# Kernel tuning notes

Hardware: AMD Instinct MI355X
Metric: run time of the kernel (lower is better)

The kernel has to match this reference:

```python
import jax, jax.numpy as jnp
import numpy as np

N, M_CHE, M_VDW, B = 20000, 20, 20, 200
H, E, NODE_IN, NCONV = 128, 20, 13, 3
CHE_CUTOFF, VDW_CUTOFF = 8.0, 12.0


def setup_inputs() -> dict:
    key = jax.random.key(0)
    ks = jax.random.split(key, 16)
    s = 0.05
    inp = {}
    inp['atoms_embed'] = jax.random.normal(ks[0], (N, NODE_IN), jnp.float32)
    inp['che_nbrs_fea'] = jax.random.uniform(ks[1], (N, M_CHE), jnp.float32, 0.5, CHE_CUTOFF * 1.1)
    inp['vdw_nbrs_fea'] = jax.random.uniform(ks[2], (N, M_VDW), jnp.float32, 0.5, VDW_CUTOFF * 1.1)
    inp['che_nbrs_idx'] = jax.random.randint(ks[3], (N, M_CHE), 0, N)
    inp['vdw_nbrs_idx'] = jax.random.randint(ks[4], (N, M_VDW), 0, N)
    inp['num_atoms'] = jnp.full((B,), N // B, dtype=jnp.int32)  # 200 crystals x 100 atoms
    inp['emb_W'] = jax.random.normal(ks[5], (NODE_IN, H), jnp.float32) * s
    inp['emb_b'] = jnp.zeros((H,), jnp.float32)
    inp['che_filter_W'] = jax.random.normal(ks[6], (NCONV, E, H), jnp.float32) * s
    inp['che_filter_b'] = jnp.zeros((NCONV, H), jnp.float32)
    inp['che_fc_W'] = jax.random.normal(ks[7], (NCONV, 3 * H, 2 * H), jnp.float32) * s
    inp['che_fc_b'] = jnp.zeros((NCONV, 2 * H), jnp.float32)
    inp['vdw_filter_W'] = jax.random.normal(ks[8], (NCONV, E, H), jnp.float32) * s
    inp['vdw_filter_b'] = jnp.zeros((NCONV, H), jnp.float32)
    inp['vdw_fc_W'] = jax.random.normal(ks[9], (NCONV, 3 * H, 2 * H), jnp.float32) * s
    inp['vdw_fc_b'] = jnp.zeros((NCONV, 2 * H), jnp.float32)
    inp['fc1_W'] = jax.random.normal(ks[10], (H, H), jnp.float32) * s
    inp['fc1_b'] = jnp.zeros((H,), jnp.float32)
    inp['out_W'] = jax.random.normal(ks[11], (H, 1), jnp.float32) * s
    inp['out_b'] = jnp.zeros((1,), jnp.float32)
    return inp


def _rbf(d, cutoff):
    # sinc-like radial basis with cosine envelope; zero beyond cutoff
    k = jnp.arange(1, E + 1, dtype=d.dtype)  # [E]
    de = d[..., None]  # [N, M, 1]
    r = jnp.where(de < cutoff, jnp.sin(de * k * (jnp.pi / cutoff)) / de, jnp.zeros((), d.dtype))
    env = 0.5 * (jnp.cos(jnp.pi * d / cutoff) + 1.0)
    return r * env[..., None]  # [N, M, E]


def _conv_half(nodes, rbf_e, idx, fW, fb, gW, gb):
    n, m = idx.shape
    edges = rbf_e @ fW + fb  # [N, M, H]
    self_fea = jnp.broadcast_to(nodes[:, None, :], (n, m, nodes.shape[1]))
    total = jnp.concatenate([self_fea, edges, nodes[idx]], axis=2)  # [N, M, 3H]
    gated = total @ gW + gb  # [N, M, 2H]
    filt, core = jnp.split(gated, 2, axis=2)
    return jnp.sum(jax.nn.sigmoid(filt) * jax.nn.softplus(core), axis=1)  # [N, H]


def reference(atoms_embed, che_nbrs_fea, che_nbrs_idx, vdw_nbrs_fea, vdw_nbrs_idx,
              num_atoms, emb_W, emb_b, che_filter_W, che_filter_b, che_fc_W, che_fc_b,
              vdw_filter_W, vdw_filter_b, vdw_fc_W, vdw_fc_b, fc1_W, fc1_b, out_W, out_b):
    nodes = atoms_embed @ emb_W + emb_b  # [N, H]
    che_rbf = _rbf(che_nbrs_fea, CHE_CUTOFF)
    vdw_rbf = _rbf(vdw_nbrs_fea, VDW_CUTOFF)
    for i in range(NCONV):
        che = _conv_half(nodes, che_rbf, che_nbrs_idx, che_filter_W[i], che_filter_b[i], che_fc_W[i], che_fc_b[i])
        vdw = _conv_half(nodes, vdw_rbf, vdw_nbrs_idx, vdw_filter_W[i], vdw_filter_b[i], vdw_fc_W[i], vdw_fc_b[i])
        nodes = jax.nn.softplus(nodes + che + vdw)
    # per-crystal mean pooling from contiguous atom ranges given by num_atoms
    ends = jnp.cumsum(num_atoms)
    seg = jnp.searchsorted(ends, jnp.arange(nodes.shape[0]), side='right')
    sums = jax.ops.segment_sum(nodes, seg, num_segments=B)
    crys = sums / num_atoms[:, None].astype(nodes.dtype)  # [B, H]
    crys = jax.nn.softplus(jax.nn.softplus(crys) @ fc1_W + fc1_b)
    predict = (crys @ out_W + out_b)[:, 0]  # [B]
    return predict
```

## Files before the change

kernel.cpp:

```cpp
#include <hip/hip_runtime.h>
#include <hip/hip_bf16.h>
#include <math.h>

#define NN 20000
#define MM 20
#define EE 20
#define HH 128
#define BB 200
#define NCONV 3
#define CHE_CUT 8.0f
#define VDW_CUT 12.0f
#define PI_F 3.14159265358979323846f
#define LOG2E_F 1.44269504088896340736f
#define LN2_F 0.69314718055994530942f

typedef __fp16 half2_t __attribute__((ext_vector_type(2)));
typedef __fp16 half4_t __attribute__((ext_vector_type(4)));
typedef _Float16 f16x8 __attribute__((ext_vector_type(8)));
typedef float f32x4 __attribute__((ext_vector_type(4)));

__device__ __forceinline__ float exp2_(float x) {
#if __has_builtin(__builtin_amdgcn_exp2f)
    return __builtin_amdgcn_exp2f(x);
#else
    return exp2f(x);
#endif
}
__device__ __forceinline__ float log2_(float x) {
#if __has_builtin(__builtin_amdgcn_logf)
    return __builtin_amdgcn_logf(x);
#else
    return log2f(x);
#endif
}
__device__ __forceinline__ float rcp_(float x) {
#if __has_builtin(__builtin_amdgcn_rcpf)
    return __builtin_amdgcn_rcpf(x);
#else
    return 1.f / x;
#endif
}
__device__ __forceinline__ float med3_(float a, float b, float c) {
#if __has_builtin(__builtin_amdgcn_fmed3f)
    return __builtin_amdgcn_fmed3f(a, b, c);
#else
    return fminf(a, fmaxf(b, c));
#endif
}
__device__ __forceinline__ float sp_(float x) {
    return (x > 15.f) ? x : LN2_F * log2_(1.f + exp2_(x * LOG2E_F));
}
__device__ __forceinline__ float fdot2_(half2_t a, half2_t b, float c) {
#if __has_builtin(__builtin_amdgcn_fdot2)
    return __builtin_amdgcn_fdot2(a, b, c, false);
#else
    return (float)a.x * (float)b.x + (float)a.y * (float)b.y + c;
#endif
}

__global__ void prep_bias(const float* __restrict__ cfb, const float* __restrict__ cgW,
                          const float* __restrict__ cgb,
                          const float* __restrict__ vfb, const float* __restrict__ vgW,
                          const float* __restrict__ vgb, float* __restrict__ bc) {
    int half = blockIdx.y;
    int l = blockIdx.z;
    int j = threadIdx.x;
    const float* fb = half ? vfb : cfb;
    const float* gW = half ? vgW : cgW;
    const float* gb = half ? vgb : cgb;
    const float* gWe = gW + ((size_t)l * 384 + 128) * 256;
    const float* brow = fb + (size_t)l * HH;
    float acc = gb[(size_t)l * 256 + j];
    for (int k = 0; k < HH; ++k) acc = fmaf(brow[k], gWe[k * 256 + j], acc);
    bc[((size_t)l * 2 + half) * 256 + j] = acc * LOG2E_F;
}

__global__ void prep_bwc(const float* __restrict__ cfW, const float* __restrict__ cgW,
                         const float* __restrict__ vfW, const float* __restrict__ vgW,
                         _Float16* __restrict__ bwc) {
    int nt = blockIdx.x;
    int half = blockIdx.y;
    int l = blockIdx.z;
    int tid = threadIdx.x;
    int k = tid >> 4, nc = tid & 15;
    int t = (nt & 7) * 16 + nc;
    int gcol = (nt >> 3) * 128 + t;
    const float* fW = half ? vfW : cfW;
    const float* gW = half ? vgW : cgW;
    const float* gWe = gW + ((size_t)l * 384 + 128) * 256;
    float val = 0.f;
    if (k < EE) {
        const float* frow = fW + ((size_t)l * EE + k) * HH;
        for (int kk = 0; kk < HH; ++kk) val = fmaf(frow[kk], gWe[kk * 256 + gcol], val);
        val *= LOG2E_F;
    }
    bwc[(((size_t)(l * 2 + half) * 16 + nt) * 64 + (k >> 3) * 16 + nc) * 8 + (k & 7)] = (_Float16)val;
}

__global__ void prep_bpk(const float* __restrict__ cgW, const float* __restrict__ vgW,
                         _Float16* __restrict__ bpk) {
    int i = blockIdx.x * 256 + threadIdx.x;
    if (i >= NCONV * 128 * 1024) return;
    int l = i >> 17;
    int rem = i & 131071;
    int k = rem >> 10;
    int c = rem & 1023;
    int half = (c >> 8) & 1;
    const float* src = half ? vgW : cgW;
    int grow = l * 384 + ((c < 512) ? k : 256 + k);
    float val = src[(size_t)grow * 256 + (c & 255)] * LOG2E_F;
    int nt = c >> 4, nc = c & 15;
    int s = k >> 5, kq = (k >> 3) & 3, j = k & 7;
    bpk[(size_t)l * 131072 + (((size_t)nt * 4 + s) * 64 + kq * 16 + nc) * 8 + j] = (_Float16)val;
}

__global__ void embed_kernel(const float* __restrict__ atoms, const float* __restrict__ W,
                             const float* __restrict__ bias, float* __restrict__ nodes,
                             _Float16* __restrict__ nodes_h) {
    int n = blockIdx.x, t = threadIdx.x;
    const float* arow = atoms + (size_t)n * 13;
    float acc = bias[t];
    #pragma unroll
    for (int k = 0; k < 13; ++k) acc = fmaf(arow[k], W[k * HH + t], acc);
    nodes[(size_t)n * HH + t] = acc;
    nodes_h[(size_t)n * HH + t] = (_Float16)acc;
}

__global__ void rbf_kernel(const float* __restrict__ che_fea, const float* __restrict__ vdw_fea,
                           _Float16* __restrict__ rfrag) {
    int i = blockIdx.x * blockDim.x + threadIdx.x;
    if (i >= 2 * NN * MM) return;
    bool isv = i >= NN * MM;
    int rem = isv ? i - NN * MM : i;
    int n = rem / MM, m = rem % MM;
    float d = isv ? vdw_fea[rem] : che_fea[rem];
    float cutoff = isv ? VDW_CUT : CHE_CUT;
    float x = d * (PI_F / cutoff);
    float s1 = sinf(x), c1 = cosf(x);
    float env = 0.5f * (c1 + 1.f);
    float scale = (d < cutoff) ? (env / d) : 0.f;
    float out[EE];
    float skm1 = 0.f, sk = s1;
    #pragma unroll
    for (int e = 0; e < EE; ++e) {
        out[e] = sk * scale;
        float nx = 2.f * c1 * sk - skm1;
        skm1 = sk; sk = nx;
    }
    _Float16* rf = rfrag + (size_t)(isv ? NN + n : n) * 640;
    f16x8 v0, v1, v2, v3;
    #pragma unroll
    for (int j = 0; j < 8; ++j) {
        v0[j] = (_Float16)out[j];
        v1[j] = (_Float16)out[8 + j];
        v2[j] = (j < 4) ? (_Float16)out[16 + j] : (_Float16)0.f;
        v3[j] = (_Float16)0.f;
    }
    if (m < 16) {
        _Float16* base = rf + m * 8;
        *(f16x8*)(base) = v0;
        *(f16x8*)(base + 128) = v1;
        *(f16x8*)(base + 256) = v2;
        *(f16x8*)(base + 384) = v3;
    } else {
        _Float16* base = rf + 512 + (m - 16) * 8;
        *(f16x8*)(base) = v0;
        *(f16x8*)(base + 32) = v1;
        *(f16x8*)(base + 64) = v2;
        *(f16x8*)(base + 96) = v3;
    }
}

__global__ __launch_bounds__(256)
void gemm_mfma(const _Float16* __restrict__ Ah, const _Float16* __restrict__ Bpk,
               half2_t* __restrict__ Spk, half2_t* __restrict__ Ypk) {
    int lane = threadIdx.x & 63;
    int wv = threadIdx.x >> 6;
    int m0 = blockIdx.x * 32;
    int la = lane & 15;
    int quad = lane >> 4;
    int k0 = quad * 8;

    f16x8 af0[4], af1[4];
    {
        const _Float16* arow = Ah + (size_t)(m0 + la) * 128 + k0;
        #pragma unroll
        for (int s = 0; s < 4; ++s) {
            af0[s] = *(const f16x8*)(arow + s * 32);
            af1[s] = *(const f16x8*)(arow + 2048 + s * 32);
        }
    }

    const f16x8* bp = (const f16x8*)Bpk;
    int ntf0 = wv * 16;
    half2_t* dst = (wv & 2) ? Ypk : Spk;
    int wbase = (wv & 1) * 128 + la;

    f16x8 fb[4], cb[4], nfb[4], ncb[4];
    #pragma unroll
    for (int s = 0; s < 4; ++s) {
        fb[s] = bp[((size_t)ntf0 * 4 + s) * 64 + lane];
        cb[s] = bp[((size_t)(ntf0 + 8) * 4 + s) * 64 + lane];
    }
    for (int p = 0; p < 8; ++p) {
        if (p < 7) {
            #pragma unroll
            for (int s = 0; s < 4; ++s) {
                nfb[s] = bp[((size_t)(ntf0 + p + 1) * 4 + s) * 64 + lane];
                ncb[s] = bp[((size_t)(ntf0 + 9 + p) * 4 + s) * 64 + lane];
            }
        }
        f32x4 a0f = {0.f, 0.f, 0.f, 0.f};
        f32x4 a0c = {0.f, 0.f, 0.f, 0.f};
        f32x4 a1f = {0.f, 0.f, 0.f, 0.f};
        f32x4 a1c = {0.f, 0.f, 0.f, 0.f};
        #pragma unroll
        for (int s = 0; s < 4; ++s) {
            a0f = __builtin_amdgcn_mfma_f32_16x16x32_f16(af0[s], fb[s], a0f, 0, 0, 0);
            a0c = __builtin_amdgcn_mfma_f32_16x16x32_f16(af0[s], cb[s], a0c, 0, 0, 0);
            a1f = __builtin_amdgcn_mfma_f32_16x16x32_f16(af1[s], fb[s], a1f, 0, 0, 0);
            a1c = __builtin_amdgcn_mfma_f32_16x16x32_f16(af1[s], cb[s], a1c, 0, 0, 0);
        }
        int row = m0 + quad * 4;
        int word = wbase + p * 16;
        #pragma unroll
        for (int i = 0; i < 4; ++i) {
            dst[(size_t)(row + i) * 256 + word] = __builtin_amdgcn_cvt_pkrtz(a0f[i], a0c[i]);
            dst[(size_t)(row + 16 + i) * 256 + word] = __builtin_amdgcn_cvt_pkrtz(a1f[i], a1c[i]);
        }
        #pragma unroll
        for (int s = 0; s < 4; ++s) { fb[s] = nfb[s]; cb[s] = ncb[s]; }
    }
}

#define G2P 260
__global__ __launch_bounds__(256, 7)
void edge_kernel(const float* __restrict__ nodes_in, float* __restrict__ nodes_out,
                 _Float16* __restrict__ nodes_h,
                 const half2_t* __restrict__ Spk, const half2_t* __restrict__ Ypk,
                 const _Float16* __restrict__ rfrag,
                 const int* __restrict__ idx_che, const int* __restrict__ idx_vdw,
                 const _Float16* __restrict__ bwc,
                 const float* __restrict__ bC) {
    __shared__ __align__(16) half2_t G2[20 * G2P];
    __shared__ float red[HH];
    int t = threadIdx.x;
    int lane = t & 63;
    int wv = t >> 6;
    int n = blockIdx.x;
    int h2 = t >> 7;
    int tc = t & 127;

    const int* idxp = h2 ? (idx_vdw + (size_t)n * MM) : (idx_che + (size_t)n * MM);
    int jx[MM];
    {
        const int4* ip = (const int4*)idxp;
        #pragma unroll
        for (int k = 0; k < 5; ++k) *(int4*)&jx[k * 4] = ip[k];
    }

    const half2_t* yb = Ypk + h2 * 128 + tc;
    half2_t y0 = yb[(size_t)jx[0] * 256];
    half2_t y1 = yb[(size_t)jx[1] * 256];
    half2_t y2 = yb[(size_t)jx[2] * 256];
    half2_t y3 = yb[(size_t)jx[3] * 256];

    half2_t spx = Spk[(size_t)n * 256 + h2 * 128 + tc];
    float old = (h2 == 0) ? nodes_in[(size_t)n * HH + tc] : 0.f;
    float sf = bC[h2 * 256 + tc] + (float)spx.x;
    float sc = bC[h2 * 256 + 128 + tc] + (float)spx.y;

    const half2_t ONE0 = {(__fp16)1.f, (__fp16)0.f};
    const half2_t ZERO1 = {(__fp16)0.f, (__fp16)1.f};
    int quad = lane >> 4;
    int cla = lane & 15;

    {
        int hw = wv >> 1;
        const _Float16* rf = rfrag + (size_t)(hw * NN + n) * 640;
        f16x8 a0 = *(const f16x8*)(rf + lane * 8);
        f16x8 a1 = {};
        if (cla < 4) a1 = *(const f16x8*)(rf + 512 + (quad * 4 + cla) * 8);
        const f16x8* bw = (const f16x8*)bwc + ((size_t)hw * 16) * 64;
        #pragma unroll
        for (int p = 0; p < 4; ++p) {
            int pg = (wv & 1) * 4 + p;
            f16x8 bf = bw[(size_t)pg * 64 + lane];
            f16x8 bcfr = bw[(size_t)(8 + pg) * 64 + lane];
            f32x4 g0f = {0.f, 0.f, 0.f, 0.f};
            f32x4 g0c = {0.f, 0.f, 0.f, 0.f};
            f32x4 g1f = {0.f, 0.f, 0.f, 0.f};
            f32x4 g1c = {0.f, 0.f, 0.f, 0.f};
            g0f = __builtin_amdgcn_mfma_f32_16x16x32_f16(a0, bf, g0f, 0, 0, 0);
            g0c = __builtin_amdgcn_mfma_f32_16x16x32_f16(a0, bcfr, g0c, 0, 0, 0);
            g1f = __builtin_amdgcn_mfma_f32_16x16x32_f16(a1, bf, g1f, 0, 0, 0);
            g1c = __builtin_amdgcn_mfma_f32_16x16x32_f16(a1, bcfr, g1c, 0, 0, 0);
            int col = pg * 16 + cla;
            half4_t w0;
            w0.x = (__fp16)0.f;
            half2_t p0 = __builtin_amdgcn_cvt_pkrtz(g0f[0], g0c[0]);
            half2_t p1 = __builtin_amdgcn_cvt_pkrtz(g0f[1], g0c[1]);
            w0.x = p0.x; w0.y = p0.y; w0.z = p1.x; w0.w = p1.y;
            *(half4_t*)&G2[(hw * 10 + quad * 2) * G2P + col * 2] = w0;
            half4_t w1;
            half2_t p2 = __builtin_amdgcn_cvt_pkrtz(g0f[2], g0c[2]);
            half2_t p3 = __builtin_amdgcn_cvt_pkrtz(g0f[3], g0c[3]);
            w1.x = p2.x; w1.y = p2.y; w1.z = p3.x; w1.w = p3.y;
            *(half4_t*)&G2[(hw * 10 + quad * 2 + 1) * G2P + col * 2] = w1;
            if (quad == 0) {
                half4_t w2;
                half2_t q0 = __builtin_amdgcn_cvt_pkrtz(g1f[0], g1c[0]);
                half2_t q1 = __builtin_amdgcn_cvt_pkrtz(g1f[1], g1c[1]);
                w2.x = q0.x; w2.y = q0.y; w2.z = q1.x; w2.w = q1.y;
                *(half4_t*)&G2[(hw * 10 + 8) * G2P + col * 2] = w2;
                half4_t w3;
                half2_t q2 = __builtin_amdgcn_cvt_pkrtz(g1f[2], g1c[2]);
                half2_t q3 = __builtin_amdgcn_cvt_pkrtz(g1f[3], g1c[3]);
                w3.x = q2.x; w3.y = q2.y; w3.z = q3.x; w3.w = q3.y;
                *(half4_t*)&G2[(hw * 10 + 9) * G2P + col * 2] = w3;
            }
        }
    }
    __syncthreads();

    float acc = 0.f;
    const half2_t* gq = G2 + (h2 * 10) * G2P + tc * 2;
    #pragma unroll
    for (int cb = 0; cb < 5; ++cb) {
        half2_t n0 = {}, n1 = {}, n2 = {}, n3 = {};
        if (cb < 4) {
            n0 = yb[(size_t)jx[cb * 4 + 4] * 256];
            n1 = yb[(size_t)jx[cb * 4 + 5] * 256];
            n2 = yb[(size_t)jx[cb * 4 + 6] * 256];
            n3 = yb[(size_t)jx[cb * 4 + 7] * 256];
        }
        half4_t gp0 = *(const half4_t*)(gq + (size_t)(2 * cb) * G2P);
        half4_t gp1 = *(const half4_t*)(gq + (size_t)(2 * cb + 1) * G2P);
        half2_t gw0 = half2_t{gp0.x, gp0.y} + y0;
        half2_t gw1 = half2_t{gp0.z, gp0.w} + y1;
        half2_t gw2 = half2_t{gp1.x, gp1.y} + y2;
        half2_t gw3 = half2_t{gp1.z, gp1.w} + y3;
        float gf0 = fdot2_(gw0, ONE0, sf), gc0 = fdot2_(gw0, ZERO1, sc);
        float gf1 = fdot2_(gw1, ONE0, sf), gc1 = fdot2_(gw1, ZERO1, sc);
        float gf2 = fdot2_(gw2, ONE0, sf), gc2 = fdot2_(gw2, ZERO1, sc);
        float gf3 = fdot2_(gw3, ONE0, sf), gc3 = fdot2_(gw3, ZERO1, sc);
        float u0 = rcp_(1.f + exp2_(-gf0));
        float u1 = rcp_(1.f + exp2_(-gf1));
        float u2 = rcp_(1.f + exp2_(-gf2));
        float u3 = rcp_(1.f + exp2_(-gf3));
        float p0 = med3_(log2_(1.f + exp2_(gc0)), gc0, 25.f);
        float p1 = med3_(log2_(1.f + exp2_(gc1)), gc1, 25.f);
        float p2 = med3_(log2_(1.f + exp2_(gc2)), gc2, 25.f);
        float p3 = med3_(log2_(1.f + exp2_(gc3)), gc3, 25.f);
        acc = fmaf(p0, u0, acc);
        acc = fmaf(p1, u1, acc);
        acc = fmaf(p2, u2, acc);
        acc = fmaf(p3, u3, acc);
        y0 = n0; y1 = n1; y2 = n2; y3 = n3;
    }
    if (h2) red[tc] = acc;
    __syncthreads();
    if (!h2) {
        float res = sp_(fmaf(acc + red[tc], LN2_F, old));
        nodes_out[(size_t)n * HH + tc] = res;
        nodes_h[(size_t)n * HH + tc] = (_Float16)res;
    }
}

__global__ void pool_kernel(const float* __restrict__ nodes, const int* __restrict__ num_atoms,
                            const float* __restrict__ fc1_W, const float* __restrict__ fc1_b,
                            const float* __restrict__ out_W, const float* __restrict__ out_b,
                            float* __restrict__ out) {
    __shared__ float sh[HH];
    __shared__ float red[HH];
    int b = blockIdx.x, t = threadIdx.x;
    int start = 0;
    for (int i = 0; i < b; ++i) start += num_atoms[i];
    int cnt = num_atoms[b];
    float sum = 0.f;
    for (int a = 0; a < cnt; ++a) sum += nodes[(size_t)(start + a) * HH + t];
    float mean = sum / (float)cnt;
    sh[t] = sp_(mean);
    __syncthreads();
    float o = fc1_b[t];
    #pragma unroll 4
    for (int k = 0; k < HH; ++k) o = fmaf(sh[k], fc1_W[k * HH + t], o);
    red[t] = sp_(o) * out_W[t];
    __syncthreads();
    if (t == 0) {
        float tot = 0.f;
        for (int k = 0; k < HH; ++k) tot += red[k];
        out[b] = tot + out_b[0];
    }
}

extern "C" void kernel_launch(void* const* d_in, const int* in_sizes, int n_in,
                              void* d_out, int out_size, void* d_ws, size_t ws_size,
                              hipStream_t stream) {
    const float* atoms_embed   = (const float*)d_in[0];
    const float* che_nbrs_fea  = (const float*)d_in[1];
    const float* vdw_nbrs_fea  = (const float*)d_in[2];
    const int*   che_nbrs_idx  = (const int*)  d_in[3];
    const int*   vdw_nbrs_idx  = (const int*)  d_in[4];
    const int*   num_atoms     = (const int*)  d_in[5];
    const float* emb_W         = (const float*)d_in[6];
    const float* emb_b         = (const float*)d_in[7];
    const float* che_filter_W  = (const float*)d_in[8];
    const float* che_filter_b  = (const float*)d_in[9];
    const float* che_fc_W      = (const float*)d_in[10];
    const float* che_fc_b      = (const float*)d_in[11];
    const float* vdw_filter_W  = (const float*)d_in[12];
    const float* vdw_filter_b  = (const float*)d_in[13];
    const float* vdw_fc_W      = (const float*)d_in[14];
    const float* vdw_fc_b      = (const float*)d_in[15];
    const float* fc1_W         = (const float*)d_in[16];
    const float* fc1_b         = (const float*)d_in[17];
    const float* out_W         = (const float*)d_in[18];
    const float* out_b         = (const float*)d_in[19];
    float* out = (float*)d_out;

    float* w = (float*)d_ws;
    float* nodesA   = w;
    float* nodesB   = nodesA + (size_t)NN * HH;
    _Float16* nodes_h = (_Float16*)(nodesB + (size_t)NN * HH);
    half2_t* Spk    = (half2_t*)(nodes_h + (size_t)NN * HH);
    half2_t* Ypk    = Spk + (size_t)NN * 256;
    _Float16* rfrag = (_Float16*)(Ypk + (size_t)NN * 256);
    _Float16* bpk   = rfrag + (size_t)2 * NN * 640;
    _Float16* bwc   = bpk + (size_t)NCONV * 131072;
    float* bc       = (float*)(bwc + (size_t)NCONV * 2 * 16 * 512);

    prep_bias<<<dim3(1, 2, NCONV), 256, 0, stream>>>(
        che_filter_b, che_fc_W, che_fc_b, vdw_filter_b, vdw_fc_W, vdw_fc_b, bc);
    prep_bwc<<<dim3(16, 2, NCONV), 512, 0, stream>>>(
        che_filter_W, che_fc_W, vdw_filter_W, vdw_fc_W, bwc);
    prep_bpk<<<(NCONV * 128 * 1024 + 255) / 256, 256, 0, stream>>>(che_fc_W, vdw_fc_W, bpk);
    embed_kernel<<<NN, HH, 0, stream>>>(atoms_embed, emb_W, emb_b, nodesA, nodes_h);
    rbf_kernel<<<(2 * NN * MM + 255) / 256, 256, 0, stream>>>(
        che_nbrs_fea, vdw_nbrs_fea, rfrag);

    float* cur = nodesA;
    float* nxt = nodesB;
    for (int l = 0; l < NCONV; ++l) {
        gemm_mfma<<<NN / 32, 256, 0, stream>>>(nodes_h, bpk + (size_t)l * 131072, Spk, Ypk);
        edge_kernel<<<NN, 256, 0, stream>>>(
            cur, nxt, nodes_h, Spk, Ypk, rfrag, che_nbrs_idx, vdw_nbrs_idx,
            bwc + (size_t)l * 2 * 16 * 512, bc + (size_t)l * 512);
        float* tmp = cur; cur = nxt; nxt = tmp;
    }

    pool_kernel<<<BB, HH, 0, stream>>>(cur, num_atoms, fc1_W, fc1_b, out_W, out_b, out);
}
```

Measured before the change: 455.4 us.

## Alias edge-kernel reduction buffer into G2 smem and raise occupancy; unroll GEMM double-buffering

The edge kernel's LDS footprint shrinks: G2 padding goes from 260 to 256 and the reduction array now aliases the G2 buffer, with an added barrier so the aliased write cannot race with earlier reads. Launch bounds rise from 7 to 8 blocks per CU so more blocks can be resident. The GEMM loop is fully unrolled into ping-pong buffers of B fragments, which removes the register copies between iterations. Dropping the G2 padding may bring back LDS bank conflicts, and the tighter launch bound may force register spills.

```diff
diff --git a/kernel.cpp b/kernel.cpp
--- a/kernel.cpp
+++ b/kernel.cpp
@@ -171,6 +171,26 @@
     }
 }
 
+#define GEMM_TILE(P, FB, CB)                                                     \
+    do {                                                                          \
+        f32x4 a0f = {0.f,0.f,0.f,0.f}, a0c = {0.f,0.f,0.f,0.f};                   \
+        f32x4 a1f = {0.f,0.f,0.f,0.f}, a1c = {0.f,0.f,0.f,0.f};                   \
+        _Pragma("unroll")                                                         \
+        for (int s = 0; s < 4; ++s) {                                             \
+            a0f = __builtin_amdgcn_mfma_f32_16x16x32_f16(af0[s], FB[s], a0f, 0, 0, 0); \
+            a0c = __builtin_amdgcn_mfma_f32_16x16x32_f16(af0[s], CB[s], a0c, 0, 0, 0); \
+            a1f = __builtin_amdgcn_mfma_f32_16x16x32_f16(af1[s], FB[s], a1f, 0, 0, 0); \
+            a1c = __builtin_amdgcn_mfma_f32_16x16x32_f16(af1[s], CB[s], a1c, 0, 0, 0); \
+        }                                                                         \
+        int row_ = m0 + quad * 4;                                                 \
+        int word_ = wbase + (P) * 16;                                             \
+        _Pragma("unroll")                                                         \
+        for (int i = 0; i < 4; ++i) {                                             \
+            dst[(size_t)(row_ + i) * 256 + word_] = __builtin_amdgcn_cvt_pkrtz(a0f[i], a0c[i]); \
+            dst[(size_t)(row_ + 16 + i) * 256 + word_] = __builtin_amdgcn_cvt_pkrtz(a1f[i], a1c[i]); \
+        }                                                                         \
+    } while (0)
+
 __global__ __launch_bounds__(256)
 void gemm_mfma(const _Float16* __restrict__ Ah, const _Float16* __restrict__ Bpk,
                half2_t* __restrict__ Spk, half2_t* __restrict__ Ypk) {
@@ -196,45 +216,34 @@
     half2_t* dst = (wv & 2) ? Ypk : Spk;
     int wbase = (wv & 1) * 128 + la;
 
-    f16x8 fb[4], cb[4], nfb[4], ncb[4];
+    f16x8 fb0[4], cb0[4], fb1[4], cb1[4];
     #pragma unroll
     for (int s = 0; s < 4; ++s) {
-        fb[s] = bp[((size_t)ntf0 * 4 + s) * 64 + lane];
-        cb[s] = bp[((size_t)(ntf0 + 8) * 4 + s) * 64 + lane];
-    }
-    for (int p = 0; p < 8; ++p) {
-        if (p < 7) {
+        fb0[s] = bp[((size_t)ntf0 * 4 + s) * 64 + lane];
+        cb0[s] = bp[((size_t)(ntf0 + 8) * 4 + s) * 64 + lane];
+    }
+    #pragma unroll
+    for (int pp = 0; pp < 4; ++pp) {
+        int p0 = 2 * pp, p1 = 2 * pp + 1;
+        #pragma unroll
+        for (int s = 0; s < 4; ++s) {
+            fb1[s] = bp[((size_t)(ntf0 + p1) * 4 + s) * 64 + lane];
+            cb1[s] = bp[((size_t)(ntf0 + 8 + p1) * 4 + s) * 64 + lane];
+        }
+        GEMM_TILE(p0, fb0, cb0);
+        if (pp < 3) {
             #pragma unroll
             for (int s = 0; s < 4; ++s) {
-                nfb[s] = bp[((size_t)(ntf0 + p + 1) * 4 + s) * 64 + lane];
-                ncb[s] = bp[((size_t)(ntf0 + 9 + p) * 4 + s) * 64 + lane];
+                fb0[s] = bp[((size_t)(ntf0 + p0 + 2) * 4 + s) * 64 + lane];
+                cb0[s] = bp[((size_t)(ntf0 + 10 + p0) * 4 + s) * 64 + lane];
             }
         }
-        f32x4 a0f = {0.f, 0.f, 0.f, 0.f};
-        f32x4 a0c = {0.f, 0.f, 0.f, 0.f};
-        f32x4 a1f = {0.f, 0.f, 0.f, 0.f};
-        f32x4 a1c = {0.f, 0.f, 0.f, 0.f};
-        #pragma unroll
-        for (int s = 0; s < 4; ++s) {
-            a0f = __builtin_amdgcn_mfma_f32_16x16x32_f16(af0[s], fb[s], a0f, 0, 0, 0);
-            a0c = __builtin_amdgcn_mfma_f32_16x16x32_f16(af0[s], cb[s], a0c, 0, 0, 0);
-            a1f = __builtin_amdgcn_mfma_f32_16x16x32_f16(af1[s], fb[s], a1f, 0, 0, 0);
-            a1c = __builtin_amdgcn_mfma_f32_16x16x32_f16(af1[s], cb[s], a1c, 0, 0, 0);
-        }
-        int row = m0 + quad * 4;
-        int word = wbase + p * 16;
-        #pragma unroll
-        for (int i = 0; i < 4; ++i) {
-            dst[(size_t)(row + i) * 256 + word] = __builtin_amdgcn_cvt_pkrtz(a0f[i], a0c[i]);
-            dst[(size_t)(row + 16 + i) * 256 + word] = __builtin_amdgcn_cvt_pkrtz(a1f[i], a1c[i]);
-        }
-        #pragma unroll
-        for (int s = 0; s < 4; ++s) { fb[s] = nfb[s]; cb[s] = ncb[s]; }
-    }
-}
-
-#define G2P 260
-__global__ __launch_bounds__(256, 7)
+        GEMM_TILE(p1, fb1, cb1);
+    }
+}
+
+#define G2P 256
+__global__ __launch_bounds__(256, 8)
 void edge_kernel(const float* __restrict__ nodes_in, float* __restrict__ nodes_out,
                  _Float16* __restrict__ nodes_h,
                  const half2_t* __restrict__ Spk, const half2_t* __restrict__ Ypk,
@@ -242,8 +251,9 @@
                  const int* __restrict__ idx_che, const int* __restrict__ idx_vdw,
                  const _Float16* __restrict__ bwc,
                  const float* __restrict__ bC) {
-    __shared__ __align__(16) half2_t G2[20 * G2P];
-    __shared__ float red[HH];
+    __shared__ __align__(16) unsigned char smem[20 * G2P * 4];
+    half2_t* G2 = (half2_t*)smem;
+    float* red = (float*)smem;
     int t = threadIdx.x;
     int lane = t & 63;
     int wv = t >> 6;
@@ -297,7 +307,6 @@
             g1c = __builtin_amdgcn_mfma_f32_16x16x32_f16(a1, bcfr, g1c, 0, 0, 0);
             int col = pg * 16 + cla;
             half4_t w0;
-            w0.x = (__fp16)0.f;
             half2_t p0 = __builtin_amdgcn_cvt_pkrtz(g0f[0], g0c[0]);
             half2_t p1 = __builtin_amdgcn_cvt_pkrtz(g0f[1], g0c[1]);
             w0.x = p0.x; w0.y = p0.y; w0.z = p1.x; w0.w = p1.y;
@@ -358,6 +367,7 @@
         acc = fmaf(p3, u3, acc);
         y0 = n0; y1 = n1; y2 = n2; y3 = n3;
     }
+    __syncthreads();
     if (h2) red[tc] = acc;
     __syncthreads();
     if (!h2) {
```

After: 448.9 us. No clear change (-1.4%).
